# Kernel tuning notes

Measured on AMD Instinct MI355X. Metric: run time of the kernel, lower is better.

## Reference

```python
import jax, jax.numpy as jnp
import numpy as np

ROPE_DIM = 64
ROPE_THETA = 10000.0
SLIDING_WINDOW = 1024
_K_MASK = jnp.finfo(jnp.bfloat16).min


def _pos_embeddings(positions, head_dim, rope_theta):
    # positions: [B, T] -> sin, cos: [B, T, head_dim]
    fraction = jnp.arange(0, head_dim, 2, dtype=jnp.float32) / head_dim
    inv_freq = 1.0 / (rope_theta ** fraction)
    sinusoid = jnp.einsum('BT,k->BTk', positions.astype(jnp.float32), inv_freq,
                          precision=jax.lax.Precision.HIGHEST)
    sin = jnp.sin(sinusoid); cos = jnp.cos(sinusoid)
    return jnp.concatenate([sin, sin], -1), jnp.concatenate([cos, cos], -1)


def _rotate_half(x):
    x1, x2 = x[..., :x.shape[-1] // 2], x[..., x.shape[-1] // 2:]
    return jnp.concatenate([-x2, x1], -1)


def _apply_rope_partial(x, sin, cos, rope_dim):
    x_rope, x_nope = x[..., :rope_dim], x[..., rope_dim:]
    sin = sin[:, :, None, :]; cos = cos[:, :, None, :]
    x_rope = x_rope * cos + _rotate_half(x_rope) * sin
    return jnp.concatenate([x_rope, x_nope], -1).astype(x.dtype)


def setup_inputs() -> dict:
    key = jax.random.key(0)
    ks = jax.random.split(key, 6)
    B, T, D = 2, 2048, 2048
    N, K, H, Hv = 16, 4, 128, 128
    S = 2048  # cache size
    sc = 0.02
    return {
        'x': jax.random.normal(ks[0], (B, T, D), jnp.float32),
        'wq': jax.random.normal(ks[1], (D, N, H), jnp.float32) * sc,
        'wk': jax.random.normal(ks[2], (D, K, H), jnp.float32) * sc,
        'wv': jax.random.normal(ks[3], (D, K, Hv), jnp.float32) * sc,
        'wo': jax.random.normal(ks[4], (N, Hv, D), jnp.float32) * sc,
        'sink_bias': jnp.zeros((N,), jnp.float32),
        'k_cache': jnp.zeros((B, S, K, H), jnp.float32),
        'v_cache': jnp.zeros((B, S, K, Hv), jnp.float32),
        'segment_ids': jnp.ones((B, T), jnp.int32),
        'cur_ind': 0,
        'start_ind': -jnp.ones((B,), jnp.int32),
    }


def reference(x, wq, wk, wv, wo, sink_bias, k_cache, v_cache,
              segment_ids, cur_ind, start_ind):
    B, T, D = x.shape
    N, H = wq.shape[1], wq.shape[2]
    K, Hv = wk.shape[1], wv.shape[2]
    n_rep = N // K
    scaling = H ** -0.5
    cur_ind = jnp.asarray(cur_ind, jnp.int32)

    q = jnp.einsum('BTD,DNH->BTNH', x, wq)
    k = jnp.einsum('BSD,DKH->BSKH', x, wk)
    v = jnp.einsum('BSD,DKV->BSKV', x, wv)

    # left pads / positions from segment ids
    left_pads = jnp.sum(jnp.cumsum(segment_ids != 0, axis=-1) == 0, -1).astype(jnp.int32)
    start = jnp.where(start_ind < 0, left_pads, start_ind)
    pos = jax.vmap(lambda row: jnp.where(row != 0,
                                         jnp.arange(T, dtype=jnp.int32) - jnp.argmax(row).astype(jnp.int32),
                                         2 ** 30))(segment_ids) + cur_ind
    sin, cos = _pos_embeddings(pos, ROPE_DIM, ROPE_THETA)
    q = _apply_rope_partial(q, sin, cos, ROPE_DIM)
    k = _apply_rope_partial(k, sin, cos, ROPE_DIM)

    # KV cache append
    kc = jax.lax.dynamic_update_slice(k_cache, k, (0, cur_ind, 0, 0))
    vc = jax.lax.dynamic_update_slice(v_cache, v, (0, cur_ind, 0, 0))
    S = kc.shape[1]

    # GQA repeat
    kr = jnp.repeat(kc[:, :, :, None, :], n_rep, axis=3).reshape(B, S, N, H)
    vr = jnp.repeat(vc[:, :, :, None, :], n_rep, axis=3).reshape(B, S, N, Hv)

    logits = jnp.einsum('BTNH,BSNH->BTNS', q, kr) * scaling

    q_pos = cur_ind + jnp.arange(T, dtype=jnp.int32)[None, :] - start[:, None]
    ts = jnp.arange(S, dtype=jnp.int32)
    kv_seg = (ts[None, :] >= start[:, None]) & (ts[None, :] < cur_ind + T)
    k_pos = ts[None, :] - start[:, None]
    causal = k_pos[:, None, :] <= q_pos[:, :, None]
    seg_mask = kv_seg[:, None, :] == segment_ids[:, :, None]
    window = k_pos[:, None, :] >= q_pos[:, :, None] - (SLIDING_WINDOW - 1)
    final_mask = causal & seg_mask & window  # [B, T, S]
    logits = jnp.where(final_mask[:, :, None, :], logits, _K_MASK)

    # attention sink bias: extra softmax slot per head
    sink = jnp.broadcast_to(sink_bias[None, None, :, None], (B, T, N, 1))
    logits = jnp.concatenate([logits, sink], axis=-1)
    weights = jax.nn.softmax(logits.astype(jnp.float32), axis=-1).astype(logits.dtype)
    weights = weights[..., :-1]

    attn = jnp.einsum('BTNS,BSNV->BTNV', weights, vr)
    return jnp.einsum('BTNV,NVD->BTD', attn, wo)
```

## Files before the change

kernel.cpp:

```cpp
#include <hip/hip_runtime.h>
#include <hip/hip_bf16.h>
#include <stdint.h>

#define BB 2
#define TT 2048
#define DD 2048
#define NHQ 16
#define KH 4
#define HD 128
#define SS 2048
#define WINDOW 1024
#define M2FIX 12.0f
#define QSC_LOG2E 0.12751751f
#define LOG2E 1.4426950408889634f
#define NLOG2F 0.4152410118609203f

typedef __attribute__((ext_vector_type(8))) short bf16x8;
typedef __attribute__((ext_vector_type(4))) float f32x4;
typedef __attribute__((ext_vector_type(16))) float f32x16;

#define MFMA16(a, b, c) __builtin_amdgcn_mfma_f32_16x16x32_bf16(a, b, c, 0, 0, 0)
#define MFMA32(a, b, c) __builtin_amdgcn_mfma_f32_32x32x16_bf16(a, b, c, 0, 0, 0)

__device__ __forceinline__ ushort f2bf(float f) {
  uint32_t u = __float_as_uint(f);
  u += 0x7FFF + ((u >> 16) & 1);
  return (ushort)(u >> 16);
}
__device__ __forceinline__ ushort f2bf_trunc(float f) {
  return (ushort)(__float_as_uint(f) >> 16);
}
__device__ __forceinline__ float bf2f(ushort h) {
  return __uint_as_float(((uint32_t)h) << 16);
}

__device__ __forceinline__ void async_copy16(const ushort* g, ushort* l) {
  __builtin_amdgcn_global_load_lds(
      (const __attribute__((address_space(1))) uint32_t*)g,
      (__attribute__((address_space(3))) uint32_t*)l, 16, 0, 0);
}

__device__ __forceinline__ void tr_tile(const float* __restrict__ in,
                                        ushort* __restrict__ out,
                                        int C, int ldo, int cx, int cy) {
  __shared__ float tile[32][33];
  int tx = threadIdx.x & 31, ty = threadIdx.x >> 5;
  int r0 = cy * 32, c0 = cx * 32;
#pragma unroll
  for (int k = 0; k < 4; k++)
    tile[ty + k * 8][tx] = in[(size_t)(r0 + ty + k * 8) * C + c0 + tx];
  __syncthreads();
#pragma unroll
  for (int k = 0; k < 4; k++)
    out[(size_t)(c0 + ty + k * 8) * ldo + r0 + tx] = f2bf(tile[tx][ty + k * 8]);
}

__global__ void prep_fused(const float* __restrict__ x, const float* __restrict__ wq,
                           const float* __restrict__ wk, const float* __restrict__ wv,
                           const float* __restrict__ wo, const int* __restrict__ seg,
                           const int* __restrict__ start_ind, ushort* __restrict__ xb,
                           ushort* __restrict__ WcatT, ushort* __restrict__ WoT,
                           int* __restrict__ meta) {
  int bz = blockIdx.x;
  int tid = threadIdx.x;
  if (bz < 2) {
    __shared__ int red[256];
    int b = bz;
    int first = TT;
    for (int t = tid; t < TT; t += 256)
      if (seg[b * TT + t] != 0) first = min(first, t);
    red[tid] = first;
    __syncthreads();
    for (int s = 128; s > 0; s >>= 1) {
      if (tid < s) red[tid] = min(red[tid], red[tid + s]);
      __syncthreads();
    }
    if (tid == 0) {
      int fi = red[0];
      int st = start_ind[b] < 0 ? fi : start_ind[b];
      meta[b * 2 + 0] = st;
      meta[b * 2 + 1] = (fi >= TT) ? 0 : fi;
    }
    return;
  }
  bz -= 2;
  if (bz < 2048) {
#pragma unroll
    for (int p = 0; p < 4; p++) {
      int i = bz * 1024 + p * 256 + tid;
      float4 v = ((const float4*)x)[i];
      ushort4 o;
      o.x = f2bf(v.x); o.y = f2bf(v.y); o.z = f2bf(v.z); o.w = f2bf(v.w);
      ((ushort4*)xb)[i] = o;
    }
    return;
  }
  bz -= 2048;
  if (bz < 4096) { tr_tile(wq, WcatT, 2048, 2048, bz & 63, bz >> 6); return; }
  bz -= 4096;
  if (bz < 1024) { tr_tile(wk, WcatT + (size_t)2048 * 2048, 512, 2048, bz & 15, bz >> 4); return; }
  bz -= 1024;
  if (bz < 1024) { tr_tile(wv, WcatT + (size_t)2560 * 2048, 512, 2048, bz & 15, bz >> 4); return; }
  bz -= 1024;
  tr_tile(wo, WoT, 2048, 2048, bz & 63, bz >> 6);
}

__global__ void transpose_v(const ushort* __restrict__ in, ushort* __restrict__ out) {
  __shared__ ushort tile[32][33];
  int mtx = blockIdx.z;
  in  += (size_t)mtx * SS * HD;
  out += (size_t)mtx * SS * HD;
  int tx = threadIdx.x & 31, ty = threadIdx.x >> 5;
  int s0 = blockIdx.x * 32, h0 = blockIdx.y * 32;
#pragma unroll
  for (int k = 0; k < 4; k++)
    tile[ty + k * 8][tx] = in[(size_t)(s0 + ty + k * 8) * HD + h0 + tx];
  __syncthreads();
#pragma unroll
  for (int k = 0; k < 4; k++) {
    int h = h0 + ty + k * 8;
    int s = s0 + tx;
    int cit = (s & 63) >> 3;
    int sout = (s & ~63) | ((cit ^ (h & 7)) << 3) | (s & 7);
    out[(size_t)h * SS + sout] = tile[tx][ty + k * 8];
  }
}

__global__ __launch_bounds__(256) void gemm_qkv(const ushort* __restrict__ A,
                                                const ushort* __restrict__ Bt,
                                                const int* __restrict__ seg,
                                                const int* __restrict__ cur_p,
                                                const int* __restrict__ meta,
                                                ushort* __restrict__ qa,
                                                ushort* __restrict__ ka,
                                                ushort* __restrict__ va) {
  const int K = DD;
  __shared__ ushort As[128 * 64];
  __shared__ ushort Bs[128 * 64];
  __shared__ float posf_s[128];
  int tid = threadIdx.x;
  int lane = tid & 63, wave = tid >> 6;
  int wr = wave >> 1, wc = wave & 1;
  int row0 = blockIdx.y * 128, col0 = blockIdx.x * 128;
  int l31 = lane & 31, khalf = lane >> 5, lx8 = l31 & 7;
  int cur = cur_p[0];

  if (tid < 128) {
    int m = row0 + tid;
    int bb = m >> 11, t = m & 2047;
    int segv = seg[m];
    int first = meta[bb * 2 + 1];
    posf_s[tid] = (segv != 0) ? (float)(t - first + cur) : 1073741824.0f;
  }

  f32x16 acc[2][2];
#pragma unroll
  for (int i = 0; i < 2; i++)
#pragma unroll
    for (int j = 0; j < 2; j++)
#pragma unroll
      for (int e = 0; e < 16; e++) acc[i][j][e] = 0.f;

  int srow = tid >> 3, scol = tid & 7;
  int ssw = (scol ^ (srow & 7)) * 8;
  const ushort* Ag = A  + (size_t)(row0 + srow) * K + ssw;
  const ushort* Bg = Bt + (size_t)(col0 + srow) * K + ssw;
  ushort* AsD = As + tid * 8;
  ushort* BsD = Bs + tid * 8;

  for (int kc = 0; kc < K; kc += 64) {
    __syncthreads();
#pragma unroll
    for (int p = 0; p < 4; p++)
      async_copy16(Ag + kc + (size_t)(p * 32) * K, AsD + p * 2048);
#pragma unroll
    for (int p = 0; p < 4; p++)
      async_copy16(Bg + kc + (size_t)(p * 32) * K, BsD + p * 2048);
    __syncthreads();
#pragma unroll
    for (int ks = 0; ks < 4; ks++) {
      bf16x8 af[2], bfm[2];
      int ch = (ks * 2 + khalf) ^ lx8;
#pragma unroll
      for (int i = 0; i < 2; i++)
        af[i] = *(const bf16x8*)(As + (wr * 64 + i * 32 + l31) * 64 + ch * 8);
#pragma unroll
      for (int j = 0; j < 2; j++)
        bfm[j] = *(const bf16x8*)(Bs + (wc * 64 + j * 32 + l31) * 64 + ch * 8);
#pragma unroll
      for (int i = 0; i < 2; i++)
#pragma unroll
        for (int j = 0; j < 2; j++)
          acc[i][j] = MFMA32(af[i], bfm[j], acc[i][j]);
    }
  }

  int cb0 = col0 + wc * 64;
  int region = (cb0 < 2048) ? 0 : (cb0 < 2560 ? 1 : 2);
  bool ropehalf = ((cb0 & 64) == 0) && (region <= 1);
  int hbase = cb0 & 64;
  float invf = exp2f(-NLOG2F * (float)l31);

#pragma unroll
  for (int i = 0; i < 2; i++) {
#pragma unroll
    for (int reg = 0; reg < 16; reg++) {
      int rloc = wr * 64 + i * 32 + (reg & 3) + 8 * (reg >> 2) + 4 * khalf;
      int m = row0 + rloc;
      int b = m >> 11, t = m & 2047;
      float v0 = acc[i][0][reg], v1 = acc[i][1][reg];
      if (ropehalf) {
        float posf = posf_s[rloc];
        float sn, cs;
        __sincosf(posf * invf, &sn, &cs);
        float n0 = v0 * cs - v1 * sn;
        v1 = v1 * cs + v0 * sn;
        v0 = n0;
      }
      if (region == 0) {
        int head = cb0 >> 7;
        size_t base = ((size_t)(b * NHQ + head) * TT + t) * HD + hbase;
        qa[base + l31]      = f2bf(v0 * QSC_LOG2E);
        qa[base + 32 + l31] = f2bf(v1 * QSC_LOG2E);
      } else if (region == 1) {
        int head = (cb0 - 2048) >> 7;
        size_t rowbase = ((size_t)(b * KH + head) * SS + t) * HD;
        int sw = t & 7;
        int c0x = hbase + l31, c1x = hbase + 32 + l31;
        ka[rowbase + ((((c0x >> 3) ^ sw) << 3) | (c0x & 7))] = f2bf(v0);
        ka[rowbase + ((((c1x >> 3) ^ sw) << 3) | (c1x & 7))] = f2bf(v1);
      } else {
        int head = (cb0 - 2560) >> 7;
        size_t base = ((size_t)(b * KH + head) * SS + t) * HD + hbase;
        va[base + l31]      = f2bf(v0);
        va[base + 32 + l31] = f2bf(v1);
      }
    }
  }
}

template <int OUT_F32>
__global__ __launch_bounds__(256) void gemm_bt(const ushort* __restrict__ A,
                                               const ushort* __restrict__ Bt,
                                               void* __restrict__ Cout,
                                               int M, int N, int K) {
  __shared__ ushort As[128 * 64];
  __shared__ ushort Bs[128 * 64];
  int tid = threadIdx.x;
  int lane = tid & 63, wave = tid >> 6;
  int wr = wave >> 1, wc = wave & 1;
  int row0 = blockIdx.y * 128, col0 = blockIdx.x * 128;
  int l31 = lane & 31, khalf = lane >> 5, lx8 = l31 & 7;

  f32x16 acc[2][2];
#pragma unroll
  for (int i = 0; i < 2; i++)
#pragma unroll
    for (int j = 0; j < 2; j++)
#pragma unroll
      for (int e = 0; e < 16; e++) acc[i][j][e] = 0.f;

  int srow = tid >> 3, scol = tid & 7;
  int ssw = (scol ^ (srow & 7)) * 8;
  const ushort* Ag = A  + (size_t)(row0 + srow) * K + ssw;
  const ushort* Bg = Bt + (size_t)(col0 + srow) * K + ssw;
  ushort* AsD = As + tid * 8;
  ushort* BsD = Bs + tid * 8;

  for (int kc = 0; kc < K; kc += 64) {
    __syncthreads();
#pragma unroll
    for (int p = 0; p < 4; p++)
      async_copy16(Ag + kc + (size_t)(p * 32) * K, AsD + p * 2048);
#pragma unroll
    for (int p = 0; p < 4; p++)
      async_copy16(Bg + kc + (size_t)(p * 32) * K, BsD + p * 2048);
    __syncthreads();
#pragma unroll
    for (int ks = 0; ks < 4; ks++) {
      bf16x8 af[2], bfm[2];
      int ch = (ks * 2 + khalf) ^ lx8;
#pragma unroll
      for (int i = 0; i < 2; i++)
        af[i] = *(const bf16x8*)(As + (wr * 64 + i * 32 + l31) * 64 + ch * 8);
#pragma unroll
      for (int j = 0; j < 2; j++)
        bfm[j] = *(const bf16x8*)(Bs + (wc * 64 + j * 32 + l31) * 64 + ch * 8);
#pragma unroll
      for (int i = 0; i < 2; i++)
#pragma unroll
        for (int j = 0; j < 2; j++)
          acc[i][j] = MFMA32(af[i], bfm[j], acc[i][j]);
    }
  }

#pragma unroll
  for (int i = 0; i < 2; i++)
#pragma unroll
    for (int reg = 0; reg < 16; reg++) {
      int r = row0 + wr * 64 + i * 32 + (reg & 3) + 8 * (reg >> 2) + 4 * khalf;
#pragma unroll
      for (int j = 0; j < 2; j++) {
        int c = col0 + wc * 64 + j * 32 + l31;
        float v = acc[i][j][reg];
        if (OUT_F32)
          ((float*)Cout)[(size_t)r * N + c] = v;
        else
          ((ushort*)Cout)[(size_t)r * N + c] = f2bf(v);
      }
    }
}

__global__ __launch_bounds__(256) void flash_attn(
    const ushort* __restrict__ qa, const ushort* __restrict__ ka,
    const ushort* __restrict__ vat, const float* __restrict__ sink_bias,
    const int* __restrict__ seg, const int* __restrict__ cur_p,
    const int* __restrict__ meta, ushort* __restrict__ Obuf) {
  __shared__ ushort Ks[64 * 128];
  __shared__ ushort VT[128 * 64];
  __shared__ ushort Ps[4 * 16 * 64];

  int bx = blockIdx.x;
  int u = bx & 255, v = bx >> 8;
  int combo = u & 31, j5 = u >> 5;
  int b = combo >> 4, n = combo & 15;
  int qt = (v == 0) ? j5 : (v == 1) ? (15 - j5) : (v == 2) ? (16 + j5) : (31 - j5);
  int kb = n >> 2;
  int t0 = qt * 64;
  int cur = cur_p[0];
  int start = meta[b * 2];

  int tid = threadIdx.x, lane = tid & 63, w = tid >> 6;
  int lcol = lane & 15, quad = lane >> 4, lx = lcol & 7;
  int t0w = t0 + w * 16;

  const ushort* qbase = qa + (size_t)(b * NHQ + n) * TT * HD;
  const ushort* kbase = ka + (size_t)(b * KH + kb) * SS * HD;
  const ushort* vtb   = vat + (size_t)(b * KH + kb) * HD * SS;

  bf16x8 qf[4];
  {
    const ushort* qrow = qbase + (size_t)(t0w + lcol) * HD + quad * 8;
#pragma unroll
    for (int c = 0; c < 4; c++) qf[c] = *(const bf16x8*)(qrow + c * 32);
  }

  int segq[4], trow[4];
#pragma unroll
  for (int r = 0; r < 4; r++) {
    trow[r] = t0w + quad * 4 + r;
    segq[r] = seg[b * TT + trow[r]];
  }
  int seg1 = __all(segq[0] == 1 && segq[1] == 1 && segq[2] == 1 && segq[3] == 1);

  f32x4 oacc[8], lacc;
#pragma unroll
  for (int ob = 0; ob < 8; ob++) { f32x4 z = {0.f, 0.f, 0.f, 0.f}; oacc[ob] = z; }
  { f32x4 z = {0.f, 0.f, 0.f, 0.f}; lacc = z; }

  bf16x8 ones;
#pragma unroll
  for (int e = 0; e < 8; e++) ones[e] = (short)0x3F80;

  ushort* KsD = Ks + tid * 8;
  ushort* VTD = VT + tid * 8;
  const ushort* KgT = kbase + tid * 8;
  const ushort* VgT = vtb + (size_t)(tid >> 3) * SS + (tid & 7) * 8;

  int lo = cur + t0 - (WINDOW - 1); if (lo < 0) lo = 0;
  int hi = cur + t0 + 63;           if (hi > SS - 1) hi = SS - 1;
  int ktlo = lo >> 6, kthi = hi >> 6;

  ushort* PsW = Ps + w * 1024;

  for (int kt = ktlo; kt <= kthi; kt++) {
    int ks0 = kt * 64;
    __syncthreads();
#pragma unroll
    for (int p = 0; p < 4; p++)
      async_copy16(KgT + (size_t)ks0 * 128 + p * 2048, KsD + p * 2048);
#pragma unroll
    for (int p = 0; p < 4; p++)
      async_copy16(VgT + ks0 + (size_t)p * 32 * SS, VTD + p * 2048);
    __syncthreads();

    bool active = (ks0 <= cur + t0w + 15) && (ks0 + 63 >= cur + t0w - (WINDOW - 1));
    if (active) {
      f32x4 sacc[4];
#pragma unroll
      for (int cb = 0; cb < 4; cb++) { f32x4 z = {0.f, 0.f, 0.f, 0.f}; sacc[cb] = z; }
#pragma unroll
      for (int c = 0; c < 4; c++) {
#pragma unroll
        for (int cb = 0; cb < 4; cb++) {
          bf16x8 kf = *(const bf16x8*)(Ks + (cb * 16 + lcol) * 128 +
                                       (((c * 4 + quad) ^ lx)) * 8);
          sacc[cb] = MFMA16(qf[c], kf, sacc[cb]);
        }
      }

      bool fast = seg1 && (ks0 >= start) && (ks0 + 63 <= cur + t0w) &&
                  (ks0 >= cur + t0w + 15 - (WINDOW - 1));
      if (fast) {
#pragma unroll
        for (int r = 0; r < 4; r++) {
          int row = quad * 4 + r;
#pragma unroll
          for (int cb = 0; cb < 4; cb++) {
            float p = exp2f(sacc[cb][r] - M2FIX);
            PsW[row * 64 + (((cb * 2 + (lcol >> 3)) ^ (row & 7)) * 8) + lx] = f2bf_trunc(p);
          }
        }
      } else {
        int sidx[4], kvseg[4];
#pragma unroll
        for (int cb = 0; cb < 4; cb++) {
          sidx[cb] = ks0 + cb * 16 + lcol;
          kvseg[cb] = (sidx[cb] >= start && sidx[cb] < cur + TT) ? 1 : 0;
        }
#pragma unroll
        for (int r = 0; r < 4; r++) {
          int row = quad * 4 + r;
          int qp = (segq[r] != 0) ? (cur + trow[r]) : (1 << 29);
#pragma unroll
          for (int cb = 0; cb < 4; cb++) {
            bool ok = (sidx[cb] <= qp) && (sidx[cb] >= qp - (WINDOW - 1)) &&
                      (kvseg[cb] == segq[r]);
            float p = ok ? exp2f(sacc[cb][r] - M2FIX) : 0.f;
            PsW[row * 64 + (((cb * 2 + (lcol >> 3)) ^ (row & 7)) * 8) + lx] = f2bf_trunc(p);
          }
        }
      }

#pragma unroll
      for (int c2 = 0; c2 < 2; c2++) {
        bf16x8 pf = *(const bf16x8*)(PsW + lcol * 64 + (((c2 * 4 + quad) ^ lx)) * 8);
#pragma unroll
        for (int ob = 0; ob < 8; ob++) {
          bf16x8 vf = *(const bf16x8*)(VT + (ob * 16 + lcol) * 64 +
                                       (((c2 * 4 + quad) ^ lx)) * 8);
          oacc[ob] = MFMA16(pf, vf, oacc[ob]);
        }
        lacc = MFMA16(pf, ones, lacc);
      }
    }
  }

  float sb = sink_bias[n];
#pragma unroll
  for (int r = 0; r < 4; r++) {
    float l = lacc[r] + exp2f(sb * LOG2E - M2FIX);
    float inv = 1.f / l;
    int t = trow[r];
    size_t base = ((size_t)(b * TT + t)) * (NHQ * HD) + n * HD;
#pragma unroll
    for (int ob = 0; ob < 8; ob++)
      Obuf[base + ob * 16 + lcol] = f2bf(oacc[ob][r] * inv);
  }
}

extern "C" void kernel_launch(void* const* d_in, const int* in_sizes, int n_in,
                              void* d_out, int out_size, void* d_ws, size_t ws_size,
                              hipStream_t stream) {
  const float* x  = (const float*)d_in[0];
  const float* wq = (const float*)d_in[1];
  const float* wk = (const float*)d_in[2];
  const float* wv = (const float*)d_in[3];
  const float* wo = (const float*)d_in[4];
  const float* sink = (const float*)d_in[5];
  const int* seg = (const int*)d_in[8];
  const int* cur = (const int*)d_in[9];
  const int* start_ind = (const int*)d_in[10];

  char* ws = (char*)d_ws;
  ushort* xb    = (ushort*)(ws + 0);
  ushort* WcatT = (ushort*)(ws + 16777216);
  ushort* WoT   = (ushort*)(ws + 29360128);
  ushort* qa    = (ushort*)(ws + 37748736);
  ushort* ka    = (ushort*)(ws + 54525952);
  ushort* va    = (ushort*)(ws + 58720256);
  ushort* vat   = (ushort*)(ws + 62914560);
  ushort* Obuf  = (ushort*)(ws + 67108864);
  int*    meta  = (int*)(ws + 83886080);

  prep_fused<<<12290, 256, 0, stream>>>(x, wq, wk, wv, wo, seg, start_ind,
                                        xb, WcatT, WoT, meta);
  gemm_qkv<<<dim3(24, 32), 256, 0, stream>>>(xb, WcatT, seg, cur, meta, qa, ka, va);
  transpose_v<<<dim3(64, 4, 8), 256, 0, stream>>>(va, vat);
  flash_attn<<<1024, 256, 0, stream>>>(qa, ka, vat, sink, seg, cur, meta, Obuf);
  gemm_bt<1><<<dim3(16, 32), 256, 0, stream>>>(Obuf, WoT, d_out, 4096, 2048, 2048);
}
```

Before: 315.9 us.

## Rewrite QKV GEMM with 256x256 tiles, double-buffered async loads and block swizzle

New measurement: 316.4 us. No clear change (+0.2%).

```diff
diff --git a/kernel.cpp b/kernel.cpp
--- a/kernel.cpp
+++ b/kernel.cpp
@@ -126,74 +126,146 @@
   }
 }
 
-__global__ __launch_bounds__(256) void gemm_qkv(const ushort* __restrict__ A,
-                                                const ushort* __restrict__ Bt,
-                                                const int* __restrict__ seg,
-                                                const int* __restrict__ cur_p,
-                                                const int* __restrict__ meta,
-                                                ushort* __restrict__ qa,
-                                                ushort* __restrict__ ka,
-                                                ushort* __restrict__ va) {
-  const int K = DD;
-  __shared__ ushort As[128 * 64];
-  __shared__ ushort Bs[128 * 64];
-  __shared__ float posf_s[128];
+__global__ __launch_bounds__(512, 2) void gemm_qkv(const ushort* __restrict__ A,
+                                                   const ushort* __restrict__ Bt,
+                                                   const int* __restrict__ seg,
+                                                   const int* __restrict__ cur_p,
+                                                   const int* __restrict__ meta,
+                                                   ushort* __restrict__ qa,
+                                                   ushort* __restrict__ ka,
+                                                   ushort* __restrict__ va) {
+  __shared__ ushort As[2][2][8192];
+  __shared__ ushort Bs[2][2][8192];
+  __shared__ float posf_s[256];
+
   int tid = threadIdx.x;
   int lane = tid & 63, wave = tid >> 6;
-  int wr = wave >> 1, wc = wave & 1;
-  int row0 = blockIdx.y * 128, col0 = blockIdx.x * 128;
-  int l31 = lane & 31, khalf = lane >> 5, lx8 = l31 & 7;
+  int wr = wave >> 2, wc = wave & 3;
+  int l31 = lane & 31, khalf = lane >> 5;
+
+  int rr = blockIdx.y * 12 + blockIdx.x;
+  int wid = (rr & 7) * 24 + (rr >> 3);
+  int by = wid / 12, bx = wid - by * 12;
+  int row0 = by * 256, col0 = bx * 256;
   int cur = cur_p[0];
 
-  if (tid < 128) {
+  if (tid < 256) {
     int m = row0 + tid;
     int bb = m >> 11, t = m & 2047;
     int segv = seg[m];
     int first = meta[bb * 2 + 1];
     posf_s[tid] = (segv != 0) ? (float)(t - first + cur) : 1073741824.0f;
   }
-
-  f32x16 acc[2][2];
-#pragma unroll
-  for (int i = 0; i < 2; i++)
+  asm volatile("s_waitcnt lgkmcnt(0)" ::: "memory");
+
+  f32x16 acc[4][2];
+#pragma unroll
+  for (int i = 0; i < 4; i++)
 #pragma unroll
     for (int j = 0; j < 2; j++)
 #pragma unroll
       for (int e = 0; e < 16; e++) acc[i][j][e] = 0.f;
 
-  int srow = tid >> 3, scol = tid & 7;
-  int ssw = (scol ^ (srow & 7)) * 8;
-  const ushort* Ag = A  + (size_t)(row0 + srow) * K + ssw;
-  const ushort* Bg = Bt + (size_t)(col0 + srow) * K + ssw;
-  ushort* AsD = As + tid * 8;
-  ushort* BsD = Bs + tid * 8;
-
-  for (int kc = 0; kc < K; kc += 64) {
-    __syncthreads();
-#pragma unroll
-    for (int p = 0; p < 4; p++)
-      async_copy16(Ag + kc + (size_t)(p * 32) * K, AsD + p * 2048);
-#pragma unroll
-    for (int p = 0; p < 4; p++)
-      async_copy16(Bg + kc + (size_t)(p * 32) * K, BsD + p * 2048);
-    __syncthreads();
-#pragma unroll
-    for (int ks = 0; ks < 4; ks++) {
-      bf16x8 af[2], bfm[2];
-      int ch = (ks * 2 + khalf) ^ lx8;
-#pragma unroll
-      for (int i = 0; i < 2; i++)
-        af[i] = *(const bf16x8*)(As + (wr * 64 + i * 32 + l31) * 64 + ch * 8);
-#pragma unroll
-      for (int j = 0; j < 2; j++)
-        bfm[j] = *(const bf16x8*)(Bs + (wc * 64 + j * 32 + l31) * 64 + ch * 8);
-#pragma unroll
-      for (int i = 0; i < 2; i++)
-#pragma unroll
-        for (int j = 0; j < 2; j++)
-          acc[i][j] = MFMA32(af[i], bfm[j], acc[i][j]);
-    }
-  }
+  int offA00, offA10, offA20, offA30, offA01, offA11, offA21, offA31;
+  int offB00, offB01, offB10, offB11;
+  {
+    int r0 = wr * 128 + l31;
+#pragma unroll
+    for (int dummy = 0; dummy < 1; dummy++) {
+      int r, c;
+      r = r0 + 0;  c = khalf;     offA00 = r * 32 + ((c ^ ((r >> 1) & 3)) * 8);
+      r = r0 + 32; c = khalf;     offA10 = r * 32 + ((c ^ ((r >> 1) & 3)) * 8);
+      r = r0 + 64; c = khalf;     offA20 = r * 32 + ((c ^ ((r >> 1) & 3)) * 8);
+      r = r0 + 96; c = khalf;     offA30 = r * 32 + ((c ^ ((r >> 1) & 3)) * 8);
+      r = r0 + 0;  c = 2 + khalf; offA01 = r * 32 + ((c ^ ((r >> 1) & 3)) * 8);
+      r = r0 + 32; c = 2 + khalf; offA11 = r * 32 + ((c ^ ((r >> 1) & 3)) * 8);
+      r = r0 + 64; c = 2 + khalf; offA21 = r * 32 + ((c ^ ((r >> 1) & 3)) * 8);
+      r = r0 + 96; c = 2 + khalf; offA31 = r * 32 + ((c ^ ((r >> 1) & 3)) * 8);
+    }
+    int rb = wc * 64 + l31;
+    int r, c;
+    r = rb + 0;  c = khalf;     offB00 = r * 32 + ((c ^ ((r >> 1) & 3)) * 8);
+    r = rb + 0;  c = 2 + khalf; offB01 = r * 32 + ((c ^ ((r >> 1) & 3)) * 8);
+    r = rb + 32; c = khalf;     offB10 = r * 32 + ((c ^ ((r >> 1) & 3)) * 8);
+    r = rb + 32; c = 2 + khalf; offB11 = r * 32 + ((c ^ ((r >> 1) & 3)) * 8);
+  }
+
+  int srow = tid >> 2;
+  int scol = ((tid & 3) ^ ((tid >> 3) & 3)) * 8;
+  const ushort* Asrc = A + (size_t)(row0 + srow) * 2048 + scol;
+  const ushort* Bsrc = Bt + (size_t)(col0 + srow) * 2048 + scol;
+
+#define STAGE(SRCP, TILE, HH, SLOT)                      \
+  do {                                                   \
+    const ushort* s_ = (SRCP) + (TILE) * 64 + (HH) * 32; \
+    ushort* d_ = (SLOT) + tid * 8;                       \
+    async_copy16(s_, d_);                                \
+    async_copy16(s_ + (size_t)128 * 2048, d_ + 4096);    \
+  } while (0)
+
+#define VMGATE asm volatile("s_waitcnt vmcnt(4)" ::: "memory")
+#define NOGATE ((void)0)
+
+  bf16x8 af0k0, af1k0, af2k0, af3k0, af0k1, af1k1, af2k1, af3k1;
+
+#define PHASE(BUF, H, JP, READA, STAGE_STMT, GATE_STMT)            \
+  do {                                                             \
+    if (READA) {                                                   \
+      const ushort* Ab_ = &As[BUF][H][0];                          \
+      af0k0 = *(const bf16x8*)(Ab_ + offA00);                      \
+      af1k0 = *(const bf16x8*)(Ab_ + offA10);                      \
+      af2k0 = *(const bf16x8*)(Ab_ + offA20);                      \
+      af3k0 = *(const bf16x8*)(Ab_ + offA30);                      \
+      af0k1 = *(const bf16x8*)(Ab_ + offA01);                      \
+      af1k1 = *(const bf16x8*)(Ab_ + offA11);                      \
+      af2k1 = *(const bf16x8*)(Ab_ + offA21);                      \
+      af3k1 = *(const bf16x8*)(Ab_ + offA31);                      \
+    }                                                              \
+    const ushort* Bb_ = &Bs[BUF][H][0];                            \
+    bf16x8 bk0_ = *(const bf16x8*)(Bb_ + ((JP) ? offB10 : offB00));\
+    bf16x8 bk1_ = *(const bf16x8*)(Bb_ + ((JP) ? offB11 : offB01));\
+    STAGE_STMT;                                                    \
+    __builtin_amdgcn_s_barrier();                                  \
+    __builtin_amdgcn_s_setprio(1);                                 \
+    acc[0][JP] = MFMA32(af0k0, bk0_, acc[0][JP]);                  \
+    acc[1][JP] = MFMA32(af1k0, bk0_, acc[1][JP]);                  \
+    acc[2][JP] = MFMA32(af2k0, bk0_, acc[2][JP]);                  \
+    acc[3][JP] = MFMA32(af3k0, bk0_, acc[3][JP]);                  \
+    acc[0][JP] = MFMA32(af0k1, bk1_, acc[0][JP]);                  \
+    acc[1][JP] = MFMA32(af1k1, bk1_, acc[1][JP]);                  \
+    acc[2][JP] = MFMA32(af2k1, bk1_, acc[2][JP]);                  \
+    acc[3][JP] = MFMA32(af3k1, bk1_, acc[3][JP]);                  \
+    __builtin_amdgcn_s_setprio(0);                                 \
+    GATE_STMT;                                                     \
+    __builtin_amdgcn_s_barrier();                                  \
+    asm volatile("" ::: "memory");                                 \
+  } while (0)
+
+  STAGE(Asrc, 0, 0, &As[0][0][0]);
+  STAGE(Bsrc, 0, 0, &Bs[0][0][0]);
+  STAGE(Asrc, 0, 1, &As[0][1][0]);
+  STAGE(Bsrc, 0, 1, &Bs[0][1][0]);
+  STAGE(Asrc, 1, 0, &As[1][0][0]);
+  STAGE(Bsrc, 1, 0, &Bs[1][0][0]);
+  asm volatile("s_waitcnt vmcnt(4)" ::: "memory");
+  __builtin_amdgcn_s_barrier();
+  asm volatile("" ::: "memory");
+
+#pragma unroll 1
+  for (int it = 0; it < 16; ++it) {
+    int t1 = 2 * it + 1;
+    int u2 = (2 * it + 2) & 31;
+    int u3 = (2 * it + 3) & 31;
+    PHASE(0, 0, 0, 1, STAGE(Asrc, t1, 1, &As[1][1][0]), NOGATE);
+    PHASE(0, 0, 1, 0, STAGE(Bsrc, t1, 1, &Bs[1][1][0]), NOGATE);
+    PHASE(0, 1, 0, 1, STAGE(Asrc, u2, 0, &As[0][0][0]), NOGATE);
+    PHASE(0, 1, 1, 0, STAGE(Bsrc, u2, 0, &Bs[0][0][0]), VMGATE);
+    PHASE(1, 0, 0, 1, STAGE(Asrc, u2, 1, &As[0][1][0]), NOGATE);
+    PHASE(1, 0, 1, 0, STAGE(Bsrc, u2, 1, &Bs[0][1][0]), NOGATE);
+    PHASE(1, 1, 0, 1, STAGE(Asrc, u3, 0, &As[1][0][0]), NOGATE);
+    PHASE(1, 1, 1, 0, STAGE(Bsrc, u3, 0, &Bs[1][0][0]), VMGATE);
+  }
+  asm volatile("s_waitcnt vmcnt(0)" ::: "memory");
 
   int cb0 = col0 + wc * 64;
   int region = (cb0 < 2048) ? 0 : (cb0 < 2560 ? 1 : 2);
@@ -202,10 +274,10 @@
   float invf = exp2f(-NLOG2F * (float)l31);
 
 #pragma unroll
-  for (int i = 0; i < 2; i++) {
+  for (int i = 0; i < 4; i++) {
 #pragma unroll
     for (int reg = 0; reg < 16; reg++) {
-      int rloc = wr * 64 + i * 32 + (reg & 3) + 8 * (reg >> 2) + 4 * khalf;
+      int rloc = wr * 128 + i * 32 + (reg & 3) + 8 * (reg >> 2) + 4 * khalf;
       int m = row0 + rloc;
       int b = m >> 11, t = m & 2047;
       float v0 = acc[i][0][reg], v1 = acc[i][1][reg];
@@ -237,6 +309,10 @@
       }
     }
   }
+#undef PHASE
+#undef STAGE
+#undef VMGATE
+#undef NOGATE
 }
 
 template <int OUT_F32>
@@ -485,7 +561,7 @@
 
   prep_fused<<<12290, 256, 0, stream>>>(x, wq, wk, wv, wo, seg, start_ind,
                                         xb, WcatT, WoT, meta);
-  gemm_qkv<<<dim3(24, 32), 256, 0, stream>>>(xb, WcatT, seg, cur, meta, qa, ka, va);
+  gemm_qkv<<<dim3(12, 16), 512, 0, stream>>>(xb, WcatT, seg, cur, meta, qa, ka, va);
   transpose_v<<<dim3(64, 4, 8), 256, 0, stream>>>(va, vat);
   flash_attn<<<1024, 256, 0, stream>>>(qa, ka, vat, sink, seg, cur, meta, Obuf);
   gemm_bt<1><<<dim3(16, 32), 256, 0, stream>>>(Obuf, WoT, d_out, 4096, 2048, 2048);
```

## Rewrite QKV GEMM with 4-stage async pipeline, 128x384 tiles, permuted RoPE columns

Applied to the files above, without the earlier changes.

After: 317.7 us. Within noise of the previous version (+0.6%).

```diff
diff --git a/kernel.cpp b/kernel.cpp
--- a/kernel.cpp
+++ b/kernel.cpp
@@ -40,9 +40,13 @@
       (__attribute__((address_space(3))) uint32_t*)l, 16, 0, 0);
 }
 
+__device__ __forceinline__ int permH(int h) {
+  return (h < 64) ? ((h & 31) * 2 + (h >> 5)) : h;
+}
+
 __device__ __forceinline__ void tr_tile(const float* __restrict__ in,
                                         ushort* __restrict__ out,
-                                        int C, int ldo, int cx, int cy) {
+                                        int C, int ldo, int cx, int cy, int perm) {
   __shared__ float tile[32][33];
   int tx = threadIdx.x & 31, ty = threadIdx.x >> 5;
   int r0 = cy * 32, c0 = cx * 32;
@@ -51,8 +55,11 @@
     tile[ty + k * 8][tx] = in[(size_t)(r0 + ty + k * 8) * C + c0 + tx];
   __syncthreads();
 #pragma unroll
-  for (int k = 0; k < 4; k++)
-    out[(size_t)(c0 + ty + k * 8) * ldo + r0 + tx] = f2bf(tile[tx][ty + k * 8]);
+  for (int k = 0; k < 4; k++) {
+    int R = c0 + ty + k * 8;
+    int R2 = perm ? ((R & ~127) | permH(R & 127)) : R;
+    out[(size_t)R2 * ldo + r0 + tx] = f2bf(tile[tx][ty + k * 8]);
+  }
 }
 
 __global__ void prep_fused(const float* __restrict__ x, const float* __restrict__ wq,
@@ -96,13 +103,13 @@
     return;
   }
   bz -= 2048;
-  if (bz < 4096) { tr_tile(wq, WcatT, 2048, 2048, bz & 63, bz >> 6); return; }
+  if (bz < 4096) { tr_tile(wq, WcatT, 2048, 2048, bz & 63, bz >> 6, 1); return; }
   bz -= 4096;
-  if (bz < 1024) { tr_tile(wk, WcatT + (size_t)2048 * 2048, 512, 2048, bz & 15, bz >> 4); return; }
+  if (bz < 1024) { tr_tile(wk, WcatT + (size_t)2048 * 2048, 512, 2048, bz & 15, bz >> 4, 1); return; }
   bz -= 1024;
-  if (bz < 1024) { tr_tile(wv, WcatT + (size_t)2560 * 2048, 512, 2048, bz & 15, bz >> 4); return; }
+  if (bz < 1024) { tr_tile(wv, WcatT + (size_t)2560 * 2048, 512, 2048, bz & 15, bz >> 4, 0); return; }
   bz -= 1024;
-  tr_tile(wo, WoT, 2048, 2048, bz & 63, bz >> 6);
+  tr_tile(wo, WoT, 2048, 2048, bz & 63, bz >> 6, 0);
 }
 
 __global__ void transpose_v(const ushort* __restrict__ in, ushort* __restrict__ out) {
@@ -126,25 +133,148 @@
   }
 }
 
-__global__ __launch_bounds__(256) void gemm_qkv(const ushort* __restrict__ A,
-                                                const ushort* __restrict__ Bt,
-                                                const int* __restrict__ seg,
-                                                const int* __restrict__ cur_p,
-                                                const int* __restrict__ meta,
-                                                ushort* __restrict__ qa,
-                                                ushort* __restrict__ ka,
-                                                ushort* __restrict__ va) {
-  const int K = DD;
-  __shared__ ushort As[128 * 64];
-  __shared__ ushort Bs[128 * 64];
-  __shared__ float posf_s[128];
+__global__ __launch_bounds__(512, 2) void gemm_qkv(const ushort* __restrict__ A,
+                                                   const ushort* __restrict__ Bt,
+                                                   const int* __restrict__ seg,
+                                                   const int* __restrict__ cur_p,
+                                                   const int* __restrict__ meta,
+                                                   ushort* __restrict__ qa,
+                                                   ushort* __restrict__ ka,
+                                                   ushort* __restrict__ va) {
+  __shared__ ushort As[4][4096];
+  __shared__ ushort Bs[4][12288];
+
   int tid = threadIdx.x;
   int lane = tid & 63, wave = tid >> 6;
-  int wr = wave >> 1, wc = wave & 1;
-  int row0 = blockIdx.y * 128, col0 = blockIdx.x * 128;
-  int l31 = lane & 31, khalf = lane >> 5, lx8 = l31 & 7;
+  int wr = wave >> 2, wc = wave & 3;
+  int l31 = lane & 31, khalf = lane >> 5;
+
+  int orig = blockIdx.x;
+  int wid = (orig & 7) * 32 + (orig >> 3);
+  int by = wid >> 3, bx = wid & 7;
+  int row0 = by * 128, col0 = bx * 384;
   int cur = cur_p[0];
 
+  f32x16 acc[2][3];
+#pragma unroll
+  for (int i = 0; i < 2; i++)
+#pragma unroll
+    for (int j = 0; j < 3; j++)
+#pragma unroll
+      for (int e = 0; e < 16; e++) acc[i][j][e] = 0.f;
+
+  int offA00, offA01, offA10, offA11;
+  int offB00, offB01, offB10, offB11, offB20, offB21;
+  {
+    int r, c;
+    r = wr * 64 + 0 + l31;
+    c = khalf;     offA00 = r * 32 + ((c ^ ((r >> 1) & 3)) * 8);
+    c = 2 + khalf; offA01 = r * 32 + ((c ^ ((r >> 1) & 3)) * 8);
+    r = wr * 64 + 32 + l31;
+    c = khalf;     offA10 = r * 32 + ((c ^ ((r >> 1) & 3)) * 8);
+    c = 2 + khalf; offA11 = r * 32 + ((c ^ ((r >> 1) & 3)) * 8);
+    r = wc * 96 + 0 + l31;
+    c = khalf;     offB00 = r * 32 + ((c ^ ((r >> 1) & 3)) * 8);
+    c = 2 + khalf; offB01 = r * 32 + ((c ^ ((r >> 1) & 3)) * 8);
+    r = wc * 96 + 32 + l31;
+    c = khalf;     offB10 = r * 32 + ((c ^ ((r >> 1) & 3)) * 8);
+    c = 2 + khalf; offB11 = r * 32 + ((c ^ ((r >> 1) & 3)) * 8);
+    r = wc * 96 + 64 + l31;
+    c = khalf;     offB20 = r * 32 + ((c ^ ((r >> 1) & 3)) * 8);
+    c = 2 + khalf; offB21 = r * 32 + ((c ^ ((r >> 1) & 3)) * 8);
+  }
+
+  int swzc = ((tid & 3) ^ ((tid >> 3) & 3)) * 8;
+  const ushort* srcA  = A  + (size_t)(row0 + (tid >> 2)) * 2048 + swzc;
+  const ushort* srcB0 = Bt + (size_t)(col0 +       (tid >> 2)) * 2048 + swzc;
+  const ushort* srcB1 = Bt + (size_t)(col0 + 128 + (tid >> 2)) * 2048 + swzc;
+  const ushort* srcB2 = Bt + (size_t)(col0 + 256 + (tid >> 2)) * 2048 + swzc;
+
+#define VMW_(N) asm volatile("s_waitcnt vmcnt(" #N ")" ::: "memory")
+#define VMW(N) VMW_(N)
+
+#define PH(SLOT, SSLOT, DOSTAGE, GATE)                                   \
+  do {                                                                   \
+    if (DOSTAGE) {                                                       \
+      async_copy16(pA,  &As[SSLOT][tid * 8]);                            \
+      async_copy16(pB0, &Bs[SSLOT][tid * 8]);                            \
+      async_copy16(pB1, &Bs[SSLOT][4096 + tid * 8]);                     \
+      async_copy16(pB2, &Bs[SSLOT][8192 + tid * 8]);                     \
+      pA += 32; pB0 += 32; pB1 += 32; pB2 += 32;                         \
+    }                                                                    \
+    VMW(GATE);                                                           \
+    __builtin_amdgcn_s_barrier();                                        \
+    asm volatile("" ::: "memory");                                       \
+    {                                                                    \
+      const ushort* Ab = &As[SLOT][0];                                   \
+      const ushort* Bb = &Bs[SLOT][0];                                   \
+      bf16x8 a0k0 = *(const bf16x8*)(Ab + offA00);                       \
+      bf16x8 a1k0 = *(const bf16x8*)(Ab + offA10);                       \
+      bf16x8 a0k1 = *(const bf16x8*)(Ab + offA01);                       \
+      bf16x8 a1k1 = *(const bf16x8*)(Ab + offA11);                       \
+      bf16x8 b0k0 = *(const bf16x8*)(Bb + offB00);                       \
+      bf16x8 b1k0 = *(const bf16x8*)(Bb + offB10);                       \
+      bf16x8 b2k0 = *(const bf16x8*)(Bb + offB20);                       \
+      bf16x8 b0k1 = *(const bf16x8*)(Bb + offB01);                       \
+      bf16x8 b1k1 = *(const bf16x8*)(Bb + offB11);                       \
+      bf16x8 b2k1 = *(const bf16x8*)(Bb + offB21);                       \
+      __builtin_amdgcn_s_setprio(1);                                     \
+      acc[0][0] = MFMA32(a0k0, b0k0, acc[0][0]);                         \
+      acc[0][1] = MFMA32(a0k0, b1k0, acc[0][1]);                         \
+      acc[0][2] = MFMA32(a0k0, b2k0, acc[0][2]);                         \
+      acc[1][0] = MFMA32(a1k0, b0k0, acc[1][0]);                         \
+      acc[1][1] = MFMA32(a1k0, b1k0, acc[1][1]);                         \
+      acc[1][2] = MFMA32(a1k0, b2k0, acc[1][2]);                         \
+      acc[0][0] = MFMA32(a0k1, b0k1, acc[0][0]);                         \
+      acc[0][1] = MFMA32(a0k1, b1k1, acc[0][1]);                         \
+      acc[0][2] = MFMA32(a0k1, b2k1, acc[0][2]);                         \
+      acc[1][0] = MFMA32(a1k1, b0k1, acc[1][0]);                         \
+      acc[1][1] = MFMA32(a1k1, b1k1, acc[1][1]);                         \
+      acc[1][2] = MFMA32(a1k1, b2k1, acc[1][2]);                         \
+      __builtin_amdgcn_s_setprio(0);                                     \
+    }                                                                    \
+    __builtin_amdgcn_s_barrier();                                        \
+    asm volatile("" ::: "memory");                                       \
+  } while (0)
+
+  async_copy16(srcA,       &As[0][tid * 8]);
+  async_copy16(srcB0,      &Bs[0][tid * 8]);
+  async_copy16(srcB1,      &Bs[0][4096 + tid * 8]);
+  async_copy16(srcB2,      &Bs[0][8192 + tid * 8]);
+  async_copy16(srcA  + 32, &As[1][tid * 8]);
+  async_copy16(srcB0 + 32, &Bs[1][tid * 8]);
+  async_copy16(srcB1 + 32, &Bs[1][4096 + tid * 8]);
+  async_copy16(srcB2 + 32, &Bs[1][8192 + tid * 8]);
+  async_copy16(srcA  + 64, &As[2][tid * 8]);
+  async_copy16(srcB0 + 64, &Bs[2][tid * 8]);
+  async_copy16(srcB1 + 64, &Bs[2][4096 + tid * 8]);
+  async_copy16(srcB2 + 64, &Bs[2][8192 + tid * 8]);
+  VMW(8);
+  __builtin_amdgcn_s_barrier();
+  asm volatile("" ::: "memory");
+
+  const ushort* pA  = srcA + 96;
+  const ushort* pB0 = srcB0 + 96;
+  const ushort* pB1 = srcB1 + 96;
+  const ushort* pB2 = srcB2 + 96;
+
+#pragma unroll 1
+  for (int it = 0; it < 15; ++it) {
+    PH(0, 3, 1, 12);
+    PH(1, 0, 1, 12);
+    PH(2, 1, 1, 12);
+    PH(3, 2, 1, 12);
+  }
+  PH(0, 3, 1, 12);
+  PH(1, 0, 0, 8);
+  PH(2, 1, 0, 4);
+  PH(3, 2, 0, 0);
+#undef PH
+#undef VMW
+#undef VMW_
+
+  __syncthreads();
+  float* posf_s = (float*)&As[0][0];
   if (tid < 128) {
     int m = row0 + tid;
     int bb = m >> 11, t = m & 2047;
@@ -152,88 +282,54 @@
     int first = meta[bb * 2 + 1];
     posf_s[tid] = (segv != 0) ? (float)(t - first + cur) : 1073741824.0f;
   }
-
-  f32x16 acc[2][2];
-#pragma unroll
-  for (int i = 0; i < 2; i++)
-#pragma unroll
-    for (int j = 0; j < 2; j++)
-#pragma unroll
-      for (int e = 0; e < 16; e++) acc[i][j][e] = 0.f;
-
-  int srow = tid >> 3, scol = tid & 7;
-  int ssw = (scol ^ (srow & 7)) * 8;
-  const ushort* Ag = A  + (size_t)(row0 + srow) * K + ssw;
-  const ushort* Bg = Bt + (size_t)(col0 + srow) * K + ssw;
-  ushort* AsD = As + tid * 8;
-  ushort* BsD = Bs + tid * 8;
-
-  for (int kc = 0; kc < K; kc += 64) {
-    __syncthreads();
-#pragma unroll
-    for (int p = 0; p < 4; p++)
-      async_copy16(Ag + kc + (size_t)(p * 32) * K, AsD + p * 2048);
-#pragma unroll
-    for (int p = 0; p < 4; p++)
-      async_copy16(Bg + kc + (size_t)(p * 32) * K, BsD + p * 2048);
-    __syncthreads();
-#pragma unroll
-    for (int ks = 0; ks < 4; ks++) {
-      bf16x8 af[2], bfm[2];
-      int ch = (ks * 2 + khalf) ^ lx8;
-#pragma unroll
-      for (int i = 0; i < 2; i++)
-        af[i] = *(const bf16x8*)(As + (wr * 64 + i * 32 + l31) * 64 + ch * 8);
-#pragma unroll
-      for (int j = 0; j < 2; j++)
-        bfm[j] = *(const bf16x8*)(Bs + (wc * 64 + j * 32 + l31) * 64 + ch * 8);
-#pragma unroll
-      for (int i = 0; i < 2; i++)
-#pragma unroll
-        for (int j = 0; j < 2; j++)
-          acc[i][j] = MFMA32(af[i], bfm[j], acc[i][j]);
-    }
-  }
-
-  int cb0 = col0 + wc * 64;
-  int region = (cb0 < 2048) ? 0 : (cb0 < 2560 ? 1 : 2);
-  bool ropehalf = ((cb0 & 64) == 0) && (region <= 1);
-  int hbase = cb0 & 64;
-  float invf = exp2f(-NLOG2F * (float)l31);
-
-#pragma unroll
-  for (int i = 0; i < 2; i++) {
+  __syncthreads();
+
+  int cbase = col0 + wc * 96;
+  float invf_t[3];
+  int rope_t[3], region_t[3], hc0_t[3], head_t[3];
+#pragma unroll
+  for (int ct = 0; ct < 3; ct++) {
+    int c0t = cbase + ct * 32;
+    int hc0 = c0t & 127;
+    int region = (c0t < 2048) ? 0 : (c0t < 2560 ? 1 : 2);
+    hc0_t[ct] = hc0;
+    region_t[ct] = region;
+    rope_t[ct] = (hc0 < 64) && (region <= 1);
+    invf_t[ct] = exp2f(-NLOG2F * (float)((hc0 + l31) >> 1));
+    head_t[ct] = (region == 0) ? (c0t >> 7)
+               : (region == 1) ? ((c0t - 2048) >> 7) : ((c0t - 2560) >> 7);
+  }
+  float sgnf = (l31 & 1) ? 1.f : -1.f;
+
+#pragma unroll
+  for (int rt = 0; rt < 2; rt++) {
 #pragma unroll
     for (int reg = 0; reg < 16; reg++) {
-      int rloc = wr * 64 + i * 32 + (reg & 3) + 8 * (reg >> 2) + 4 * khalf;
+      int rloc = wr * 64 + rt * 32 + (reg & 3) + 8 * (reg >> 2) + 4 * khalf;
       int m = row0 + rloc;
       int b = m >> 11, t = m & 2047;
-      float v0 = acc[i][0][reg], v1 = acc[i][1][reg];
-      if (ropehalf) {
-        float posf = posf_s[rloc];
-        float sn, cs;
-        __sincosf(posf * invf, &sn, &cs);
-        float n0 = v0 * cs - v1 * sn;
-        v1 = v1 * cs + v0 * sn;
-        v0 = n0;
-      }
-      if (region == 0) {
-        int head = cb0 >> 7;
-        size_t base = ((size_t)(b * NHQ + head) * TT + t) * HD + hbase;
-        qa[base + l31]      = f2bf(v0 * QSC_LOG2E);
-        qa[base + 32 + l31] = f2bf(v1 * QSC_LOG2E);
-      } else if (region == 1) {
-        int head = (cb0 - 2048) >> 7;
-        size_t rowbase = ((size_t)(b * KH + head) * SS + t) * HD;
-        int sw = t & 7;
-        int c0x = hbase + l31, c1x = hbase + 32 + l31;
-        ka[rowbase + ((((c0x >> 3) ^ sw) << 3) | (c0x & 7))] = f2bf(v0);
-        ka[rowbase + ((((c1x >> 3) ^ sw) << 3) | (c1x & 7))] = f2bf(v1);
-      } else {
-        int head = (cb0 - 2560) >> 7;
-        size_t base = ((size_t)(b * KH + head) * SS + t) * HD + hbase;
-        va[base + l31]      = f2bf(v0);
-        va[base + 32 + l31] = f2bf(v1);
+      float posf = posf_s[rloc];
+#pragma unroll
+      for (int ct = 0; ct < 3; ct++) {
+        float v = acc[rt][ct][reg];
+        if (rope_t[ct]) {
+          float other = __shfl_xor(v, 1, 64);
+          float sn, cs;
+          __sincosf(posf * invf_t[ct], &sn, &cs);
+          v = v * cs + sgnf * sn * other;
+        }
+        int hc = hc0_t[ct] + l31;
+        if (region_t[ct] == 0) {
+          size_t base = ((size_t)(b * NHQ + head_t[ct]) * TT + t) * HD;
+          qa[base + hc] = f2bf(v * QSC_LOG2E);
+        } else if (region_t[ct] == 1) {
+          size_t rowbase = ((size_t)(b * KH + head_t[ct]) * SS + t) * HD;
+          int sw = t & 7;
+          ka[rowbase + ((((hc >> 3) ^ sw) << 3) | (hc & 7))] = f2bf(v);
+        } else {
+          size_t base = ((size_t)(b * KH + head_t[ct]) * SS + t) * HD;
+          va[base + hc] = f2bf(v);
+        }
       }
     }
   }
@@ -485,7 +581,7 @@
 
   prep_fused<<<12290, 256, 0, stream>>>(x, wq, wk, wv, wo, seg, start_ind,
                                         xb, WcatT, WoT, meta);
-  gemm_qkv<<<dim3(24, 32), 256, 0, stream>>>(xb, WcatT, seg, cur, meta, qa, ka, va);
+  gemm_qkv<<<dim3(256), 512, 0, stream>>>(xb, WcatT, seg, cur, meta, qa, ka, va);
   transpose_v<<<dim3(64, 4, 8), 256, 0, stream>>>(va, vat);
   flash_attn<<<1024, 256, 0, stream>>>(qa, ka, vat, sink, seg, cur, meta, Obuf);
   gemm_bt<1><<<dim3(16, 32), 256, 0, stream>>>(Obuf, WoT, d_out, 4096, 2048, 2048);
```
